# Kernel optimization log

Hardware: AMD Instinct MI355X
Metric: run time of the kernel (lower is better)

## Reference

```python
import jax, jax.numpy as jnp
import numpy as np

B, T, V, E, H, L = 128, 256, 32000, 512, 512, 4
PAD_ID = 0


def setup_inputs() -> dict:
    key = jax.random.key(0)
    ks = jax.random.split(key, 12)
    s = 1.0 / np.sqrt(H)
    emb = jax.random.normal(ks[1], (V, E), jnp.float32) * 0.02
    emb = emb.at[PAD_ID].set(0.0)  # padding_idx row is zero
    return {
        "enc_input": jax.random.randint(ks[0], (B, T), 0, V, dtype=jnp.int32),
        "emb": emb,
        # NOTE: single StackLSTMCell shared by both directions (as in BiRecurrent)
        "W_ih": jax.random.normal(ks[2], (L, 4 * H, E), jnp.float32) * s,
        "W_hh": jax.random.normal(ks[3], (L, 4 * H, H), jnp.float32) * s,
        "b_ih": jax.random.normal(ks[4], (L, 4 * H), jnp.float32) * 0.01,
        "b_hh": jax.random.normal(ks[5], (L, 4 * H), jnp.float32) * 0.01,
        "out_W": jax.random.normal(ks[6], (512, 2 * H), jnp.float32) * s,
        "out_b": jax.random.normal(ks[7], (512,), jnp.float32) * 0.01,
        "hid_W": jax.random.normal(ks[8], (512, 2 * H), jnp.float32) * s,
        "hid_b": jax.random.normal(ks[9], (512,), jnp.float32) * 0.01,
        "cell_W": jax.random.normal(ks[10], (512, 2 * H), jnp.float32) * s,
        "cell_b": jax.random.normal(ks[11], (512,), jnp.float32) * 0.01,
    }


def _run_direction(xs, W_ih, W_hh, b_ih, b_hh):
    # xs: [T, B, E]; stacked residual LSTM unrolled over time via scan
    n_layers = W_ih.shape[0]
    hdim = W_hh.shape[2]
    bsz = xs.shape[1]
    h0 = jnp.zeros((n_layers, bsz, hdim), xs.dtype)
    c0 = jnp.zeros((n_layers, bsz, hdim), xs.dtype)

    def step(carry, x_t):
        h, c = carry
        inp = x_t
        nh, nc = [], []
        for l in range(n_layers):
            gates = inp @ W_ih[l].T + b_ih[l] + h[l] @ W_hh[l].T + b_hh[l]
            i, f, g, o = jnp.split(gates, 4, axis=-1)  # torch LSTMCell gate order
            ci = jax.nn.sigmoid(f) * c[l] + jax.nn.sigmoid(i) * jnp.tanh(g)
            hi = jax.nn.sigmoid(o) * jnp.tanh(ci)
            inp = hi + inp  # residual: input dim == hidden dim at every layer
            nh.append(hi)
            nc.append(ci)
        return (jnp.stack(nh), jnp.stack(nc)), inp

    (hT, cT), outs = jax.lax.scan(step, (h0, c0), xs)
    return outs, hT, cT  # outs: [T,B,H]; hT,cT: [L,B,H]


def reference(enc_input, emb, W_ih, W_hh, b_ih, b_hh,
              out_W, out_b, hid_W, hid_b, cell_W, cell_b):
    x = jax.nn.relu(emb[enc_input])          # [B,T,E]
    xs = jnp.transpose(x, (1, 0, 2))          # [T,B,E]
    fo, fh, fc = _run_direction(xs, W_ih, W_hh, b_ih, b_hh)
    ro, rh, rc = _run_direction(xs[::-1], W_ih, W_hh, b_ih, b_hh)
    ro = ro[::-1]
    out = jnp.concatenate([fo, ro], axis=-1)  # [T,B,2H]
    out = jnp.transpose(out, (1, 0, 2)) @ out_W.T + out_b   # [B,T,512]
    hidden = jnp.concatenate([fh, rh], axis=-1) @ hid_W.T + hid_b  # [L,B,512]
    cell = jnp.concatenate([fc, rc], axis=-1) @ cell_W.T + cell_b  # [L,B,512]
    return out, hidden, cell
```

## Files before the change

### kernel.cpp

```cpp
#include <hip/hip_runtime.h>

typedef _Float16 f16;
typedef f16  f16x8 __attribute__((ext_vector_type(8)));
typedef float f32x4 __attribute__((ext_vector_type(4)));
typedef unsigned long long u64;

#define OFF_XF  0ull
#define OFF_XR  67108864ull
#define OFF_WP  134217728ull
#define OFF_WO  150994944ull
#define OFF_WH  152043520ull
#define OFF_WC  153092096ull
#define OFF_BC  154140672ull
#define OFF_HB  154173440ull
#define OFF_HT  154697728ull
#define OFF_CT  156794880ull
#define OFF_CNT 158892032ull

__device__ __forceinline__ float sigm(float x) { return 1.0f / (1.0f + expf(-x)); }

__device__ __forceinline__ f16x8 cvt8(const float* p) {
    float4 a0 = *(const float4*)p;
    float4 a1 = *(const float4*)(p + 4);
    f16x8 r;
    r[0]=(f16)a0.x; r[1]=(f16)a0.y; r[2]=(f16)a0.z; r[3]=(f16)a0.w;
    r[4]=(f16)a1.x; r[5]=(f16)a1.y; r[6]=(f16)a1.z; r[7]=(f16)a1.w;
    return r;
}

__global__ __launch_bounds__(256) void prep_pack(
    const float* __restrict__ Wih, const float* __restrict__ Whh,
    const float* __restrict__ bih, const float* __restrict__ bhh,
    const float* __restrict__ oW, const float* __restrict__ hW, const float* __restrict__ cW,
    f16* __restrict__ Wp, f16* __restrict__ Wo, f16* __restrict__ Wh, f16* __restrict__ Wc,
    float* __restrict__ bc, int* __restrict__ cnt)
{
    const int blk = blockIdx.x, tid = threadIdx.x;
    if (blk < 8192) {
        const int l = blk >> 11, p = blk & 2047;
        const int cb = p >> 6, gate = (p >> 4) & 3, j = p & 15;
        const int orig = gate*512 + cb*16 + j;
        const int swz = (p & 7) << 3;
        const float* si = Wih + ((size_t)(l*2048 + orig) << 9);
        const float* sh = Whh + ((size_t)(l*2048 + orig) << 9);
        f16* d = Wp + ((size_t)(l*2048 + p) << 10);
        for (int k = tid; k < 1024; k += 256)
            d[k ^ swz] = (f16)((k < 512) ? si[k] : sh[k - 512]);
    } else if (blk < 9728) {
        const int which = (blk - 8192) >> 9;
        const int n = (blk - 8192) & 511;
        const float* s = which == 0 ? oW : (which == 1 ? hW : cW);
        f16* d = which == 0 ? Wo : (which == 1 ? Wh : Wc);
        for (int k = tid; k < 1024; k += 256)
            d[((size_t)n << 10) + k] = (f16)s[((size_t)n << 10) + k];
    } else if (blk == 9728) {
        for (int i = tid; i < 8192; i += 256) {
            const int l = i >> 11, p = i & 2047;
            const int cb = p >> 6, gate = (p >> 4) & 3, j = p & 15;
            const int orig = l*2048 + gate*512 + cb*16 + j;
            bc[i] = bih[orig] + bhh[orig];
        }
    } else {
        for (int i = tid; i < 4096; i += 256) cnt[i] = 0;
    }
}

__global__ __launch_bounds__(256) void embed_relu(
    const int* __restrict__ ids, const float* __restrict__ emb,
    float* __restrict__ Xf, float* __restrict__ Xr)
{
    const int blk = blockIdx.x;
    const int b = blk >> 8, t = blk & 255;
    const int id = ids[b*256 + t];
    float2 v = *((const float2*)(emb + ((size_t)id << 9)) + threadIdx.x);
    v.x = fmaxf(v.x, 0.f); v.y = fmaxf(v.y, 0.f);
    const size_t e2 = (size_t)threadIdx.x * 2;
    *(float2*)(Xf + (((size_t)t*128 + b) << 9) + e2) = v;
    *(float2*)(Xr + (((size_t)(255 - t)*128 + b) << 9) + e2) = v;
}

__global__ __launch_bounds__(256, 1) void lstm_layer(
    const int l,
    const f16* __restrict__ Wp, const float* __restrict__ bc,
    float* __restrict__ Xf, float* __restrict__ Xr,
    f16* __restrict__ hbuf, float* __restrict__ hT, float* __restrict__ cT,
    int* __restrict__ cnt)
{
    extern __shared__ char smem[];
    f16*   Wlds  = (f16*)smem;
    float* Gs    = (float*)(smem + 131072);
    float* biasS = (float*)(smem + 131072 + 16640);

    const int tid  = threadIdx.x;
    const int blk  = blockIdx.x;
    const int dir  = blk >> 6;
    const int half = (blk >> 5) & 1;
    const int cb   = blk & 31;
    const int w    = tid >> 6;
    const int ln15 = tid & 15;
    const int kgrp = ((tid & 63) >> 4) << 3;

    {
        const float4* src = (const float4*)(Wp + ((size_t)(l*2048 + cb*64) << 10));
        float4* dst = (float4*)Wlds;
        for (int i = tid; i < 8192; i += 256) dst[i] = src[i];
        if (tid < 64) biasS[tid] = bc[l*2048 + cb*64 + tid];
    }
    __syncthreads();

    float* X = dir ? Xr : Xf;
    f16* hb = hbuf + (size_t)dir * 131072;
    int* cp = cnt + (((l*2 + dir)*2 + half) << 8);

    const int arow = half*64 + w*16 + ln15;
    const int swz  = (ln15 & 7) << 3;

    const int erow = tid >> 2;
    const int eb   = half*64 + erow;
    const int ecl  = (tid & 3) << 2;
    const int ecol = cb*16 + ecl;

    float creg[4] = {0.f, 0.f, 0.f, 0.f};
    float4 xdef = {0.f, 0.f, 0.f, 0.f};

    for (int t = 0; t < 256; ++t) {
        if (t > 0) {
            if (tid == 0) {
                int g = 0;
                while (__hip_atomic_load(cp + (t - 1), __ATOMIC_ACQUIRE, __HIP_MEMORY_SCOPE_AGENT) < 32) {
                    __builtin_amdgcn_s_sleep(1);
                    if (++g > 32768) break;
                }
            }
            __syncthreads();
            *(float4*)(X + ((size_t)(t - 1) << 16) + ((size_t)eb << 9) + ecol) = xdef;
        }

        f32x4 acc[4] = {{0,0,0,0},{0,0,0,0},{0,0,0,0},{0,0,0,0}};
        const float* xrow = X + ((size_t)t << 16) + ((size_t)arow << 9);

        #pragma unroll 4
        for (int ks = 0; ks < 16; ++ks) {
            const int ko = (ks << 5) + kgrp;
            const f16x8 af = cvt8(xrow + ko);
            #pragma unroll
            for (int ct = 0; ct < 4; ++ct) {
                const f16x8 bf = *(const f16x8*)(Wlds + ((ct*16 + ln15) << 10) + (ko ^ swz));
                acc[ct] = __builtin_amdgcn_mfma_f32_16x16x32_f16(af, bf, acc[ct], 0, 0, 0);
            }
        }
        if (t > 0) {
            const f16* hrow = hb + ((size_t)((t & 1) ^ 1) << 16) + ((size_t)arow << 9);
            #pragma unroll 4
            for (int ks = 0; ks < 16; ++ks) {
                const int koh = (ks << 5) + kgrp;
                u64* hp = (u64*)(hrow + koh);
                union { u64 q[2]; f16x8 v; } uu;
                uu.q[0] = __hip_atomic_load(hp,     __ATOMIC_RELAXED, __HIP_MEMORY_SCOPE_AGENT);
                uu.q[1] = __hip_atomic_load(hp + 1, __ATOMIC_RELAXED, __HIP_MEMORY_SCOPE_AGENT);
                const int ko = 512 + koh;
                #pragma unroll
                for (int ct = 0; ct < 4; ++ct) {
                    const f16x8 bf = *(const f16x8*)(Wlds + ((ct*16 + ln15) << 10) + (ko ^ swz));
                    acc[ct] = __builtin_amdgcn_mfma_f32_16x16x32_f16(uu.v, bf, acc[ct], 0, 0, 0);
                }
            }
        }

        const int grow = w*16 + (((tid & 63) >> 4) << 2);
        #pragma unroll
        for (int ct = 0; ct < 4; ++ct)
            #pragma unroll
            for (int r = 0; r < 4; ++r)
                Gs[(grow + r)*65 + ct*16 + ln15] = acc[ct][r];
        __syncthreads();

        float hq[4];
        #pragma unroll
        for (int j2 = 0; j2 < 4; ++j2) {
            const int col = ecl + j2;
            const float gi = Gs[erow*65 + col     ] + biasS[col];
            const float gf = Gs[erow*65 + col + 16] + biasS[col + 16];
            const float gg = Gs[erow*65 + col + 32] + biasS[col + 32];
            const float go = Gs[erow*65 + col + 48] + biasS[col + 48];
            const float cn = sigm(gf)*creg[j2] + sigm(gi)*tanhf(gg);
            const float hv = sigm(go)*tanhf(cn);
            creg[j2] = cn;
            hq[j2] = hv;
        }
        const float4 xold = *(const float4*)(X + ((size_t)t << 16) + ((size_t)eb << 9) + ecol);
        xdef.x = xold.x + hq[0];
        xdef.y = xold.y + hq[1];
        xdef.z = xold.z + hq[2];
        xdef.w = xold.w + hq[3];

        union { u64 q; f16 h4[4]; } hu;
        hu.h4[0]=(f16)hq[0]; hu.h4[1]=(f16)hq[1]; hu.h4[2]=(f16)hq[2]; hu.h4[3]=(f16)hq[3];
        __hip_atomic_store((u64*)(hb + ((size_t)(t & 1) << 16) + ((size_t)eb << 9) + ecol), hu.q,
                           __ATOMIC_RELAXED, __HIP_MEMORY_SCOPE_AGENT);
        if (t == 255) {
            const size_t o = (((size_t)(l*2 + dir)*128 + eb) << 9) + ecol;
            #pragma unroll
            for (int j2 = 0; j2 < 4; ++j2) { hT[o + j2] = hq[j2]; cT[o + j2] = creg[j2]; }
        }
        __syncthreads();
        if (tid == 0)
            __hip_atomic_fetch_add(cp + t, 1, __ATOMIC_RELEASE, __HIP_MEMORY_SCOPE_AGENT);
    }

    if (tid == 0) {
        int g = 0;
        while (__hip_atomic_load(cp + 255, __ATOMIC_ACQUIRE, __HIP_MEMORY_SCOPE_AGENT) < 32) {
            __builtin_amdgcn_s_sleep(1);
            if (++g > 32768) break;
        }
    }
    __syncthreads();
    *(float4*)(X + ((size_t)255 << 16) + ((size_t)eb << 9) + ecol) = xdef;
}

__global__ __launch_bounds__(256) void proj_out(
    const float* __restrict__ Xf, const float* __restrict__ Xr,
    const f16* __restrict__ Wo, const float* __restrict__ ob,
    float* __restrict__ out)
{
    const int blk = blockIdx.x;
    const int mb = (blk >> 3) << 6;
    const int nb = (blk & 7) << 6;
    const int w = threadIdx.x >> 6, ln15 = threadIdx.x & 15;
    const int kgrp = ((threadIdx.x & 63) >> 4) << 3;
    const int m = mb + w*16 + ln15;
    const int t = m & 255, b = m >> 8;
    const float* af_ = Xf + (((size_t)t*128 + b) << 9);
    const float* ar_ = Xr + (((size_t)(255 - t)*128 + b) << 9);
    f32x4 acc[4] = {{0,0,0,0},{0,0,0,0},{0,0,0,0},{0,0,0,0}};
    #pragma unroll 2
    for (int ks = 0; ks < 32; ++ks) {
        const int ko = (ks << 5) + kgrp;
        const f16x8 af = cvt8(ks < 16 ? af_ + ko : ar_ + (ko - 512));
        #pragma unroll
        for (int ct = 0; ct < 4; ++ct) {
            const int n = nb + ct*16 + ln15;
            const f16x8 bf = *(const f16x8*)(Wo + ((size_t)n << 10) + ko);
            acc[ct] = __builtin_amdgcn_mfma_f32_16x16x32_f16(af, bf, acc[ct], 0, 0, 0);
        }
    }
    const int r0 = mb + w*16 + (((threadIdx.x & 63) >> 4) << 2);
    #pragma unroll
    for (int ct = 0; ct < 4; ++ct) {
        const int n = nb + ct*16 + ln15;
        const float bb = ob[n];
        #pragma unroll
        for (int r = 0; r < 4; ++r)
            out[((size_t)(r0 + r) << 9) + n] = acc[ct][r] + bb;
    }
}

__global__ __launch_bounds__(256) void proj_state(
    const float* __restrict__ hT, const float* __restrict__ cT,
    const f16* __restrict__ Wh, const f16* __restrict__ Wc,
    const float* __restrict__ hb_, const float* __restrict__ cb_,
    float* __restrict__ out)
{
    const int blk = blockIdx.x;
    const int z = blk >> 6;
    const int sub = blk & 63;
    const int mb = (sub >> 3) << 6;
    const int nb = (sub & 7) << 6;
    const int w = threadIdx.x >> 6, ln15 = threadIdx.x & 15;
    const int kgrp = ((threadIdx.x & 63) >> 4) << 3;
    const int m = mb + w*16 + ln15;
    const int l = m >> 7, b = m & 127;
    const float* A = z ? cT : hT;
    const f16*  W  = z ? Wc : Wh;
    const float* bi = z ? cb_ : hb_;
    const float* a0 = A + (((size_t)(l*2 + 0)*128 + b) << 9);
    const float* a1 = A + (((size_t)(l*2 + 1)*128 + b) << 9);
    f32x4 acc[4] = {{0,0,0,0},{0,0,0,0},{0,0,0,0},{0,0,0,0}};
    for (int ks = 0; ks < 32; ++ks) {
        const int ko = (ks << 5) + kgrp;
        const f16x8 af = cvt8(ks < 16 ? a0 + ko : a1 + (ko - 512));
        #pragma unroll
        for (int ct = 0; ct < 4; ++ct) {
            const int n = nb + ct*16 + ln15;
            const f16x8 bf = *(const f16x8*)(W + ((size_t)n << 10) + ko);
            acc[ct] = __builtin_amdgcn_mfma_f32_16x16x32_f16(af, bf, acc[ct], 0, 0, 0);
        }
    }
    float* o = out + (size_t)z * 262144;
    const int r0 = mb + w*16 + (((threadIdx.x & 63) >> 4) << 2);
    #pragma unroll
    for (int ct = 0; ct < 4; ++ct) {
        const int n = nb + ct*16 + ln15;
        const float bb = bi[n];
        #pragma unroll
        for (int r = 0; r < 4; ++r)
            o[((size_t)(r0 + r) << 9) + n] = acc[ct][r] + bb;
    }
}

extern "C" void kernel_launch(void* const* d_in, const int* in_sizes, int n_in,
                              void* d_out, int out_size, void* d_ws, size_t ws_size,
                              hipStream_t stream)
{
    const int*   enc  = (const int*)d_in[0];
    const float* emb  = (const float*)d_in[1];
    const float* Wih  = (const float*)d_in[2];
    const float* Whh  = (const float*)d_in[3];
    const float* bih  = (const float*)d_in[4];
    const float* bhh  = (const float*)d_in[5];
    const float* oW   = (const float*)d_in[6];
    const float* obv  = (const float*)d_in[7];
    const float* hW   = (const float*)d_in[8];
    const float* hbv  = (const float*)d_in[9];
    const float* cW   = (const float*)d_in[10];
    const float* cbv  = (const float*)d_in[11];
    float* out = (float*)d_out;
    char* ws = (char*)d_ws;

    float* Xf = (float*)(ws + OFF_XF);
    float* Xr = (float*)(ws + OFF_XR);
    f16* Wp   = (f16*)(ws + OFF_WP);
    f16* Wo   = (f16*)(ws + OFF_WO);
    f16* Wh   = (f16*)(ws + OFF_WH);
    f16* Wc   = (f16*)(ws + OFF_WC);
    float* bc = (float*)(ws + OFF_BC);
    f16* hb   = (f16*)(ws + OFF_HB);
    float* hT = (float*)(ws + OFF_HT);
    float* cT = (float*)(ws + OFF_CT);
    int* cnt  = (int*)(ws + OFF_CNT);

    hipFuncSetAttribute((const void*)lstm_layer,
                        hipFuncAttributeMaxDynamicSharedMemorySize, 147968);

    prep_pack<<<9730, 256, 0, stream>>>(Wih, Whh, bih, bhh, oW, hW, cW,
                                        Wp, Wo, Wh, Wc, bc, cnt);
    embed_relu<<<32768, 256, 0, stream>>>(enc, emb, Xf, Xr);
    for (int l = 0; l < 4; ++l)
        lstm_layer<<<128, 256, 147968, stream>>>(l, Wp, bc, Xf, Xr, hb, hT, cT, cnt);
    proj_out<<<4096, 256, 0, stream>>>(Xf, Xr, Wo, obv, out);
    proj_state<<<128, 256, 0, stream>>>(hT, cT, Wh, Wc, hbv, cbv, out + 16777216);
}
```

Measured before the change: 13.68 ms.

## Restructure LSTM step with 32x32 MFMA, prepacked fragments, and all-thread polling

The recurrent kernel now uses 32x32x16 MFMA tiles with weights prepacked into per-lane fragment order, which removes the XOR swizzle and reduces LDS reads per MFMA. All h loads are issued up front, before the input GEMM, to hide global latency. Each thread spin-waits on the step counter itself with relaxed atomics instead of one thread waiting and then a block barrier. The activations switch to fast __expf-based sigmoid/tanh, and conversions use packed cvt_pkrtz. The relaxed ordering and the approximate math risk correctness and visibility issues in exchange for lower per-step latency.

Result: slower. 20.48 ms (+49.7%).

```diff
diff --git a/kernel.cpp b/kernel.cpp
--- a/kernel.cpp
+++ b/kernel.cpp
@@ -2,7 +2,9 @@
 
 typedef _Float16 f16;
 typedef f16  f16x8 __attribute__((ext_vector_type(8)));
+typedef __fp16 h16x2 __attribute__((ext_vector_type(2)));
 typedef float f32x4 __attribute__((ext_vector_type(4)));
+typedef float f32x16 __attribute__((ext_vector_type(16)));
 typedef unsigned long long u64;
 
 #define OFF_XF  0ull
@@ -17,43 +19,55 @@
 #define OFF_CT  156794880ull
 #define OFF_CNT 158892032ull
 
-__device__ __forceinline__ float sigm(float x) { return 1.0f / (1.0f + expf(-x)); }
+__device__ __forceinline__ float sigm(float x) { return 1.0f / (1.0f + __expf(-x)); }
+__device__ __forceinline__ float ftanh(float x) { return 1.0f - 2.0f / (__expf(2.0f * x) + 1.0f); }
 
 __device__ __forceinline__ f16x8 cvt8(const float* p) {
     float4 a0 = *(const float4*)p;
     float4 a1 = *(const float4*)(p + 4);
-    f16x8 r;
-    r[0]=(f16)a0.x; r[1]=(f16)a0.y; r[2]=(f16)a0.z; r[3]=(f16)a0.w;
-    r[4]=(f16)a1.x; r[5]=(f16)a1.y; r[6]=(f16)a1.z; r[7]=(f16)a1.w;
-    return r;
-}
-
-__global__ __launch_bounds__(256) void prep_pack(
-    const float* __restrict__ Wih, const float* __restrict__ Whh,
+    union { f16x8 v; h16x2 h[4]; } u;
+    u.h[0] = __builtin_amdgcn_cvt_pkrtz(a0.x, a0.y);
+    u.h[1] = __builtin_amdgcn_cvt_pkrtz(a0.z, a0.w);
+    u.h[2] = __builtin_amdgcn_cvt_pkrtz(a1.x, a1.y);
+    u.h[3] = __builtin_amdgcn_cvt_pkrtz(a1.z, a1.w);
+    return u.v;
+}
+
+__global__ __launch_bounds__(256) void prep_w(
+    const float* __restrict__ Wih, const float* __restrict__ Whh, f16* __restrict__ Wp)
+{
+    const int l = blockIdx.x >> 5, cb = blockIdx.x & 31;
+    f16* dst = Wp + (size_t)blockIdx.x * 65536;
+    for (int g = threadIdx.x; g < 8192; g += 256) {
+        const int ct = g >> 12;
+        const int r  = g & 4095;
+        const int f  = r >> 6;
+        const int ln = r & 63;
+        const int q  = ct*32 + (ln & 31);
+        const int orig = (q >> 4)*512 + cb*16 + (q & 15);
+        const int k0 = ((f >> 5) << 9) + (f & 31)*16 + ((ln >> 5) << 3);
+        const float* src = (k0 < 512)
+            ? Wih + (((size_t)(l*2048 + orig)) << 9) + k0
+            : Whh + (((size_t)(l*2048 + orig)) << 9) + (k0 - 512);
+        *(f16x8*)(dst + (size_t)g * 8) = cvt8(src);
+    }
+}
+
+__global__ __launch_bounds__(256) void prep_misc(
     const float* __restrict__ bih, const float* __restrict__ bhh,
     const float* __restrict__ oW, const float* __restrict__ hW, const float* __restrict__ cW,
-    f16* __restrict__ Wp, f16* __restrict__ Wo, f16* __restrict__ Wh, f16* __restrict__ Wc,
+    f16* __restrict__ Wo, f16* __restrict__ Wh, f16* __restrict__ Wc,
     float* __restrict__ bc, int* __restrict__ cnt)
 {
     const int blk = blockIdx.x, tid = threadIdx.x;
-    if (blk < 8192) {
-        const int l = blk >> 11, p = blk & 2047;
-        const int cb = p >> 6, gate = (p >> 4) & 3, j = p & 15;
-        const int orig = gate*512 + cb*16 + j;
-        const int swz = (p & 7) << 3;
-        const float* si = Wih + ((size_t)(l*2048 + orig) << 9);
-        const float* sh = Whh + ((size_t)(l*2048 + orig) << 9);
-        f16* d = Wp + ((size_t)(l*2048 + p) << 10);
-        for (int k = tid; k < 1024; k += 256)
-            d[k ^ swz] = (f16)((k < 512) ? si[k] : sh[k - 512]);
-    } else if (blk < 9728) {
-        const int which = (blk - 8192) >> 9;
-        const int n = (blk - 8192) & 511;
+    if (blk < 1536) {
+        const int which = blk >> 9;
+        const int n = blk & 511;
         const float* s = which == 0 ? oW : (which == 1 ? hW : cW);
         f16* d = which == 0 ? Wo : (which == 1 ? Wh : Wc);
         for (int k = tid; k < 1024; k += 256)
             d[((size_t)n << 10) + k] = (f16)s[((size_t)n << 10) + k];
-    } else if (blk == 9728) {
+    } else if (blk == 1536) {
         for (int i = tid; i < 8192; i += 256) {
             const int l = i >> 11, p = i & 2047;
             const int cb = p >> 6, gate = (p >> 4) & 3, j = p & 15;
@@ -87,136 +101,133 @@
     int* __restrict__ cnt)
 {
     extern __shared__ char smem[];
-    f16*   Wlds  = (f16*)smem;
-    float* Gs    = (float*)(smem + 131072);
-    float* biasS = (float*)(smem + 131072 + 16640);
-
-    const int tid  = threadIdx.x;
-    const int blk  = blockIdx.x;
-    const int dir  = blk >> 6;
-    const int half = (blk >> 5) & 1;
-    const int cb   = blk & 31;
-    const int w    = tid >> 6;
-    const int ln15 = tid & 15;
-    const int kgrp = ((tid & 63) >> 4) << 3;
+    f16*   Wlds = (f16*)smem;
+    float* Gs   = (float*)(smem + 131072);
+
+    const int tid = threadIdx.x;
+    const int b   = blockIdx.x;
+    const int g2  = (b >> 1) & 3;
+    const int cb  = ((b >> 3) << 1) | (b & 1);
+    const int dir = g2 >> 1;
+    const int half= g2 & 1;
+
+    const int w   = tid >> 6;
+    const int rt  = w >> 1, ct = w & 1;
+    const int ln  = tid & 63;
+    const int l31 = ln & 31;
+    const int hi  = ln >> 5;
 
     {
-        const float4* src = (const float4*)(Wp + ((size_t)(l*2048 + cb*64) << 10));
+        const float4* src = (const float4*)(Wp + (size_t)(l*32 + cb) * 65536);
         float4* dst = (float4*)Wlds;
         for (int i = tid; i < 8192; i += 256) dst[i] = src[i];
-        if (tid < 64) biasS[tid] = bc[l*2048 + cb*64 + tid];
-    }
-    __syncthreads();
+    }
 
     float* X = dir ? Xr : Xf;
     f16* hb = hbuf + (size_t)dir * 131072;
     int* cp = cnt + (((l*2 + dir)*2 + half) << 8);
 
-    const int arow = half*64 + w*16 + ln15;
-    const int swz  = (ln15 & 7) << 3;
-
-    const int erow = tid >> 2;
-    const int eb   = half*64 + erow;
-    const int ecl  = (tid & 3) << 2;
-    const int ecol = cb*16 + ecl;
+    const int arow = half*64 + rt*32 + l31;
+    const int kb0  = hi << 3;
+    const f16* wbase = Wlds + (ct << 15);
+
+    const int jl   = tid & 15;
+    const int rb   = (tid >> 4) << 2;
+    const int erow = half*64 + rb;
+    const int ecol = cb*16 + jl;
+    const float bi_ = bc[l*2048 + cb*64 +      jl];
+    const float bf_ = bc[l*2048 + cb*64 + 16 + jl];
+    const float bg_ = bc[l*2048 + cb*64 + 32 + jl];
+    const float bo_ = bc[l*2048 + cb*64 + 48 + jl];
 
     float creg[4] = {0.f, 0.f, 0.f, 0.f};
-    float4 xdef = {0.f, 0.f, 0.f, 0.f};
+    float xdef[4] = {0.f, 0.f, 0.f, 0.f};
+
+    __syncthreads();
 
     for (int t = 0; t < 256; ++t) {
         if (t > 0) {
-            if (tid == 0) {
-                int g = 0;
-                while (__hip_atomic_load(cp + (t - 1), __ATOMIC_ACQUIRE, __HIP_MEMORY_SCOPE_AGENT) < 32) {
-                    __builtin_amdgcn_s_sleep(1);
-                    if (++g > 32768) break;
+            int gd = 0;
+            while (__hip_atomic_load(cp + (t - 1), __ATOMIC_RELAXED, __HIP_MEMORY_SCOPE_AGENT) < 32) {
+                __builtin_amdgcn_s_sleep(2);
+                if (++gd > (1 << 16)) break;
+            }
+            __builtin_amdgcn_sched_barrier(0);
+            float* xw = X + (((size_t)(t - 1)) << 16) + (((size_t)erow) << 9) + ecol;
+            xw[0] = xdef[0]; xw[512] = xdef[1]; xw[1024] = xdef[2]; xw[1536] = xdef[3];
+        }
+
+        f32x16 acc = {};
+        f16x8 uu[32];
+        if (t > 0) {
+            const f16* hrow = hb + (((size_t)((t - 1) & 1)) << 16) + (((size_t)arow) << 9);
+            #pragma unroll
+            for (int ks = 0; ks < 32; ++ks) {
+                const u64* hp = (const u64*)(hrow + ks*16 + kb0);
+                union { u64 q[2]; f16x8 v; } uv;
+                uv.q[0] = __hip_atomic_load(hp,     __ATOMIC_RELAXED, __HIP_MEMORY_SCOPE_AGENT);
+                uv.q[1] = __hip_atomic_load(hp + 1, __ATOMIC_RELAXED, __HIP_MEMORY_SCOPE_AGENT);
+                uu[ks] = uv.v;
+            }
+        }
+        const float* xrow = X + (((size_t)t) << 16) + (((size_t)arow) << 9);
+        #pragma unroll
+        for (int ks = 0; ks < 32; ++ks) {
+            f16x8 af = cvt8(xrow + ks*16 + kb0);
+            f16x8 bf = *(const f16x8*)(wbase + ((ks) << 9) + (ln << 3));
+            acc = __builtin_amdgcn_mfma_f32_32x32x16_f16(af, bf, acc, 0, 0, 0);
+        }
+        if (t > 0) {
+            #pragma unroll
+            for (int ks = 0; ks < 32; ++ks) {
+                f16x8 bf = *(const f16x8*)(wbase + ((32 + ks) << 9) + (ln << 3));
+                acc = __builtin_amdgcn_mfma_f32_32x32x16_f16(uu[ks], bf, acc, 0, 0, 0);
+            }
+        }
+        {
+            const int grow0 = rt*32 + 4*hi;
+            const int q = ct*32 + l31;
+            #pragma unroll
+            for (int r = 0; r < 16; ++r)
+                Gs[(grow0 + (r & 3) + 8*(r >> 2))*68 + q] = acc[r];
+        }
+        __syncthreads();
+        {
+            const float* xo = X + (((size_t)t) << 16) + (((size_t)erow) << 9) + ecol;
+            #pragma unroll
+            for (int rr = 0; rr < 4; ++rr) {
+                const float gi = Gs[(rb + rr)*68 +      jl] + bi_;
+                const float gf = Gs[(rb + rr)*68 + 16 + jl] + bf_;
+                const float gg = Gs[(rb + rr)*68 + 32 + jl] + bg_;
+                const float go = Gs[(rb + rr)*68 + 48 + jl] + bo_;
+                const float cn = sigm(gf)*creg[rr] + sigm(gi)*ftanh(gg);
+                const float hv = sigm(go)*ftanh(cn);
+                creg[rr] = cn;
+                xdef[rr] = xo[(size_t)rr << 9] + hv;
+                union { f16 h; unsigned short u; } cu; cu.h = (f16)hv;
+                __hip_atomic_store(
+                    (unsigned short*)(hb + (((size_t)(t & 1)) << 16) + (((size_t)(erow + rr)) << 9) + ecol),
+                    cu.u, __ATOMIC_RELAXED, __HIP_MEMORY_SCOPE_AGENT);
+                if (t == 255) {
+                    const size_t o = (((size_t)(l*2 + dir)*128 + erow + rr) << 9) + ecol;
+                    hT[o] = hv; cT[o] = cn;
                 }
             }
-            __syncthreads();
-            *(float4*)(X + ((size_t)(t - 1) << 16) + ((size_t)eb << 9) + ecol) = xdef;
-        }
-
-        f32x4 acc[4] = {{0,0,0,0},{0,0,0,0},{0,0,0,0},{0,0,0,0}};
-        const float* xrow = X + ((size_t)t << 16) + ((size_t)arow << 9);
-
-        #pragma unroll 4
-        for (int ks = 0; ks < 16; ++ks) {
-            const int ko = (ks << 5) + kgrp;
-            const f16x8 af = cvt8(xrow + ko);
-            #pragma unroll
-            for (int ct = 0; ct < 4; ++ct) {
-                const f16x8 bf = *(const f16x8*)(Wlds + ((ct*16 + ln15) << 10) + (ko ^ swz));
-                acc[ct] = __builtin_amdgcn_mfma_f32_16x16x32_f16(af, bf, acc[ct], 0, 0, 0);
-            }
-        }
-        if (t > 0) {
-            const f16* hrow = hb + ((size_t)((t & 1) ^ 1) << 16) + ((size_t)arow << 9);
-            #pragma unroll 4
-            for (int ks = 0; ks < 16; ++ks) {
-                const int koh = (ks << 5) + kgrp;
-                u64* hp = (u64*)(hrow + koh);
-                union { u64 q[2]; f16x8 v; } uu;
-                uu.q[0] = __hip_atomic_load(hp,     __ATOMIC_RELAXED, __HIP_MEMORY_SCOPE_AGENT);
-                uu.q[1] = __hip_atomic_load(hp + 1, __ATOMIC_RELAXED, __HIP_MEMORY_SCOPE_AGENT);
-                const int ko = 512 + koh;
-                #pragma unroll
-                for (int ct = 0; ct < 4; ++ct) {
-                    const f16x8 bf = *(const f16x8*)(Wlds + ((ct*16 + ln15) << 10) + (ko ^ swz));
-                    acc[ct] = __builtin_amdgcn_mfma_f32_16x16x32_f16(uu.v, bf, acc[ct], 0, 0, 0);
-                }
-            }
-        }
-
-        const int grow = w*16 + (((tid & 63) >> 4) << 2);
-        #pragma unroll
-        for (int ct = 0; ct < 4; ++ct)
-            #pragma unroll
-            for (int r = 0; r < 4; ++r)
-                Gs[(grow + r)*65 + ct*16 + ln15] = acc[ct][r];
-        __syncthreads();
-
-        float hq[4];
-        #pragma unroll
-        for (int j2 = 0; j2 < 4; ++j2) {
-            const int col = ecl + j2;
-            const float gi = Gs[erow*65 + col     ] + biasS[col];
-            const float gf = Gs[erow*65 + col + 16] + biasS[col + 16];
-            const float gg = Gs[erow*65 + col + 32] + biasS[col + 32];
-            const float go = Gs[erow*65 + col + 48] + biasS[col + 48];
-            const float cn = sigm(gf)*creg[j2] + sigm(gi)*tanhf(gg);
-            const float hv = sigm(go)*tanhf(cn);
-            creg[j2] = cn;
-            hq[j2] = hv;
-        }
-        const float4 xold = *(const float4*)(X + ((size_t)t << 16) + ((size_t)eb << 9) + ecol);
-        xdef.x = xold.x + hq[0];
-        xdef.y = xold.y + hq[1];
-        xdef.z = xold.z + hq[2];
-        xdef.w = xold.w + hq[3];
-
-        union { u64 q; f16 h4[4]; } hu;
-        hu.h4[0]=(f16)hq[0]; hu.h4[1]=(f16)hq[1]; hu.h4[2]=(f16)hq[2]; hu.h4[3]=(f16)hq[3];
-        __hip_atomic_store((u64*)(hb + ((size_t)(t & 1) << 16) + ((size_t)eb << 9) + ecol), hu.q,
-                           __ATOMIC_RELAXED, __HIP_MEMORY_SCOPE_AGENT);
-        if (t == 255) {
-            const size_t o = (((size_t)(l*2 + dir)*128 + eb) << 9) + ecol;
-            #pragma unroll
-            for (int j2 = 0; j2 < 4; ++j2) { hT[o + j2] = hq[j2]; cT[o + j2] = creg[j2]; }
         }
         __syncthreads();
         if (tid == 0)
-            __hip_atomic_fetch_add(cp + t, 1, __ATOMIC_RELEASE, __HIP_MEMORY_SCOPE_AGENT);
-    }
-
-    if (tid == 0) {
-        int g = 0;
-        while (__hip_atomic_load(cp + 255, __ATOMIC_ACQUIRE, __HIP_MEMORY_SCOPE_AGENT) < 32) {
-            __builtin_amdgcn_s_sleep(1);
-            if (++g > 32768) break;
-        }
-    }
-    __syncthreads();
-    *(float4*)(X + ((size_t)255 << 16) + ((size_t)eb << 9) + ecol) = xdef;
+            __hip_atomic_fetch_add(cp + t, 1, __ATOMIC_RELAXED, __HIP_MEMORY_SCOPE_AGENT);
+    }
+
+    {
+        int gd = 0;
+        while (__hip_atomic_load(cp + 255, __ATOMIC_RELAXED, __HIP_MEMORY_SCOPE_AGENT) < 32) {
+            __builtin_amdgcn_s_sleep(2);
+            if (++gd > (1 << 16)) break;
+        }
+        float* xw = X + (((size_t)255) << 16) + (((size_t)erow) << 9) + ecol;
+        xw[0] = xdef[0]; xw[512] = xdef[1]; xw[1024] = xdef[2]; xw[1536] = xdef[3];
+    }
 }
 
 __global__ __launch_bounds__(256) void proj_out(
@@ -239,20 +250,20 @@
         const int ko = (ks << 5) + kgrp;
         const f16x8 af = cvt8(ks < 16 ? af_ + ko : ar_ + (ko - 512));
         #pragma unroll
-        for (int ct = 0; ct < 4; ++ct) {
-            const int n = nb + ct*16 + ln15;
+        for (int ctn = 0; ctn < 4; ++ctn) {
+            const int n = nb + ctn*16 + ln15;
             const f16x8 bf = *(const f16x8*)(Wo + ((size_t)n << 10) + ko);
-            acc[ct] = __builtin_amdgcn_mfma_f32_16x16x32_f16(af, bf, acc[ct], 0, 0, 0);
+            acc[ctn] = __builtin_amdgcn_mfma_f32_16x16x32_f16(af, bf, acc[ctn], 0, 0, 0);
         }
     }
     const int r0 = mb + w*16 + (((threadIdx.x & 63) >> 4) << 2);
     #pragma unroll
-    for (int ct = 0; ct < 4; ++ct) {
-        const int n = nb + ct*16 + ln15;
+    for (int ctn = 0; ctn < 4; ++ctn) {
+        const int n = nb + ctn*16 + ln15;
         const float bb = ob[n];
         #pragma unroll
         for (int r = 0; r < 4; ++r)
-            out[((size_t)(r0 + r) << 9) + n] = acc[ct][r] + bb;
+            out[((size_t)(r0 + r) << 9) + n] = acc[ctn][r] + bb;
     }
 }
 
@@ -281,21 +292,21 @@
         const int ko = (ks << 5) + kgrp;
         const f16x8 af = cvt8(ks < 16 ? a0 + ko : a1 + (ko - 512));
         #pragma unroll
-        for (int ct = 0; ct < 4; ++ct) {
-            const int n = nb + ct*16 + ln15;
+        for (int ctn = 0; ctn < 4; ++ctn) {
+            const int n = nb + ctn*16 + ln15;
             const f16x8 bf = *(const f16x8*)(W + ((size_t)n << 10) + ko);
-            acc[ct] = __builtin_amdgcn_mfma_f32_16x16x32_f16(af, bf, acc[ct], 0, 0, 0);
+            acc[ctn] = __builtin_amdgcn_mfma_f32_16x16x32_f16(af, bf, acc[ctn], 0, 0, 0);
         }
     }
     float* o = out + (size_t)z * 262144;
     const int r0 = mb + w*16 + (((threadIdx.x & 63) >> 4) << 2);
     #pragma unroll
-    for (int ct = 0; ct < 4; ++ct) {
-        const int n = nb + ct*16 + ln15;
+    for (int ctn = 0; ctn < 4; ++ctn) {
+        const int n = nb + ctn*16 + ln15;
         const float bb = bi[n];
         #pragma unroll
         for (int r = 0; r < 4; ++r)
-            o[((size_t)(r0 + r) << 9) + n] = acc[ct][r] + bb;
+            o[((size_t)(r0 + r) << 9) + n] = acc[ctn][r] + bb;
     }
 }
 
@@ -330,14 +341,14 @@
     float* cT = (float*)(ws + OFF_CT);
     int* cnt  = (int*)(ws + OFF_CNT);
 
-    hipFuncSetAttribute((const void*)lstm_layer,
-                        hipFuncAttributeMaxDynamicSharedMemorySize, 147968);
-
-    prep_pack<<<9730, 256, 0, stream>>>(Wih, Whh, bih, bhh, oW, hW, cW,
-                                        Wp, Wo, Wh, Wc, bc, cnt);
+    (void)hipFuncSetAttribute((const void*)lstm_layer,
+                              hipFuncAttributeMaxDynamicSharedMemorySize, 148480);
+
+    prep_w<<<128, 256, 0, stream>>>(Wih, Whh, Wp);
+    prep_misc<<<1538, 256, 0, stream>>>(bih, bhh, oW, hW, cW, Wo, Wh, Wc, bc, cnt);
     embed_relu<<<32768, 256, 0, stream>>>(enc, emb, Xf, Xr);
     for (int l = 0; l < 4; ++l)
-        lstm_layer<<<128, 256, 147968, stream>>>(l, Wp, bc, Xf, Xr, hb, hT, cT, cnt);
+        lstm_layer<<<128, 256, 148480, stream>>>(l, Wp, bc, Xf, Xr, hb, hT, cT, cnt);
     proj_out<<<4096, 256, 0, stream>>>(Xf, Xr, Wo, obv, out);
     proj_state<<<128, 256, 0, stream>>>(hT, cT, Wh, Wc, hbv, cbv, out + 16777216);
 }
```
